# Kernel tuning notes

Hardware: AMD Instinct MI355X
Metric: run time of the kernel (lower is better)

The kernel has to match this reference:

```python
import jax, jax.numpy as jnp
import numpy as np

V, D, H, L, B, T = 32000, 1024, 16, 4, 2, 2048
DH = D // H
F = 4 * D
EPS = 1e-5


def setup_inputs() -> dict:
    key = jax.random.key(0)
    ks = jax.random.split(key, 16)
    s = 0.02
    n = lambda k, shape: (jax.random.normal(k, shape, jnp.float32) * s)
    inp = {
        "idx": jax.random.randint(ks[0], (B, T), 0, V, dtype=jnp.int64),
        "tok_emb": n(ks[1], (V, D)),
        "pos_emb": n(ks[2], (1, T, D)),
        # per-layer stacked params; Linear weights stored as (in, out)
        "Wq": n(ks[3], (L, D, D)), "bq": jnp.zeros((L, D)),
        "Wk": n(ks[4], (L, D, D)), "bk": jnp.zeros((L, D)),
        "Wv": n(ks[5], (L, D, D)), "bv": jnp.zeros((L, D)),
        "Wo": n(ks[6], (L, D, D)), "bo": jnp.zeros((L, D)),
        "ln1_g": jnp.ones((L, D)), "ln1_b": jnp.zeros((L, D)),
        "W1": n(ks[7], (L, D, F)), "b1": jnp.zeros((L, F)),
        "W2": n(ks[8], (L, F, D)), "b2": jnp.zeros((L, D)),
        "ln2_g": jnp.ones((L, D)), "ln2_b": jnp.zeros((L, D)),
        "lnf_g": jnp.ones((D,)), "lnf_b": jnp.zeros((D,)),
        "lm_W": n(ks[9], (D, V)),
    }
    return inp


def _ln(x, g, b):
    m = jnp.mean(x, axis=-1, keepdims=True)
    v = jnp.mean(jnp.square(x - m), axis=-1, keepdims=True)
    return (x - m) * jax.lax.rsqrt(v + EPS) * g + b


def _band_attn(x, Wq, bq, Wk, bk, Wv, bv, Wo, bo):
    # width-3 causal band: query t attends to keys {t, t-1, t-2}
    b_, t_, _ = x.shape
    q = (x @ Wq + bq).reshape(b_, t_, H, DH)
    k = (x @ Wk + bk).reshape(b_, t_, H, DH)
    v = (x @ Wv + bv).reshape(b_, t_, H, DH)

    def shift(a, o):  # align key at position t-o with query t
        return jnp.pad(a, ((0, 0), (o, 0), (0, 0), (0, 0)))[:, :t_]

    ks_ = jnp.stack([shift(k, o) for o in range(3)], axis=-2)  # (B,T,H,3,DH)
    vs_ = jnp.stack([shift(v, o) for o in range(3)], axis=-2)
    scale = 1.0 / np.sqrt(DH)
    scores = jnp.einsum('bthd,bthod->btho', q, ks_) * scale       # (B,T,H,3)
    pos = jnp.arange(t_)[None, :, None, None]
    off = jnp.arange(3)[None, None, None, :]
    scores = jnp.where(pos >= off, scores, -jnp.inf)
    p = jax.nn.softmax(scores, axis=-1)
    y = jnp.einsum('btho,bthod->bthd', p, vs_).reshape(b_, t_, D)
    return y @ Wo + bo


def reference(idx, tok_emb, pos_emb, Wq, bq, Wk, bk, Wv, bv, Wo, bo,
              ln1_g, ln1_b, W1, b1, W2, b2, ln2_g, ln2_b, lnf_g, lnf_b, lm_W):
    t_ = idx.shape[1]
    x = tok_emb[idx] + pos_emb[:, :t_, :]
    for i in range(L):
        h = _ln(x, ln1_g[i], ln1_b[i])
        x = x + _band_attn(h, Wq[i], bq[i], Wk[i], bk[i], Wv[i], bv[i], Wo[i], bo[i])
        h = _ln(x, ln2_g[i], ln2_b[i])
        h = jax.nn.gelu(h @ W1[i] + b1[i], approximate=False) @ W2[i] + b2[i]
        x = x + h
    x = _ln(x, lnf_g, lnf_b)
    logits = x @ lm_W
    return logits
```

## Files before the change

kernel.cpp:

```cpp
#include <hip/hip_runtime.h>
#include <cstdint>
#include <cstddef>

#define MROWS   4096
#define TSEQ    2048
#define DMODEL  1024
#define NHEAD   16
#define FFN     4096
#define NVOCAB  32000
#define NLAYER  4

typedef float  f32x4  __attribute__((ext_vector_type(4)));
typedef __bf16 bf16x8 __attribute__((ext_vector_type(8)));

#define VMCNT(n) asm volatile("s_waitcnt vmcnt(" #n ")" ::: "memory")

__device__ __forceinline__ unsigned short f2bf(float f) {
    unsigned u = __builtin_bit_cast(unsigned, f);
    u += 0x7fffu + ((u >> 16) & 1u);
    return (unsigned short)(u >> 16);
}
__device__ __forceinline__ float bf2f(unsigned short u) {
    return __builtin_bit_cast(float, (unsigned)u << 16);
}

__device__ __forceinline__ float gelu_exact(float v) {
    return 0.5f * v * (1.0f + erff(v * 0.7071067811865476f));
}

__global__ __launch_bounds__(256) void embed_kernel(const int* __restrict__ idx,
                                                    const float* __restrict__ tok,
                                                    const float* __restrict__ pos,
                                                    float* __restrict__ x) {
    int row = blockIdx.x, tid = threadIdx.x;
    int token = idx[row];
    int t = row & (TSEQ - 1);
    float4 a = ((const float4*)(tok + (size_t)token * DMODEL))[tid];
    float4 p = ((const float4*)(pos + (size_t)t * DMODEL))[tid];
    a.x += p.x; a.y += p.y; a.z += p.z; a.w += p.w;
    ((float4*)(x + (size_t)row * DMODEL))[tid] = a;
}

__global__ __launch_bounds__(256) void ln_kernel(const float* __restrict__ x,
                                                 const float* __restrict__ g,
                                                 const float* __restrict__ b,
                                                 unsigned short* __restrict__ out) {
    int row = blockIdx.x, tid = threadIdx.x;
    float4 v = ((const float4*)(x + (size_t)row * DMODEL))[tid];
    float s1 = v.x + v.y + v.z + v.w;
    float s2 = v.x * v.x + v.y * v.y + v.z * v.z + v.w * v.w;
    for (int s = 32; s; s >>= 1) { s1 += __shfl_xor(s1, s); s2 += __shfl_xor(s2, s); }
    __shared__ float red[8];
    int lane = tid & 63, w = tid >> 6;
    if (lane == 0) { red[w] = s1; red[4 + w] = s2; }
    __syncthreads();
    s1 = red[0] + red[1] + red[2] + red[3];
    s2 = red[4] + red[5] + red[6] + red[7];
    float mean = s1 * (1.0f / DMODEL);
    float var  = s2 * (1.0f / DMODEL) - mean * mean;
    float rs   = rsqrtf(var + 1e-5f);
    float4 gv = ((const float4*)g)[tid];
    float4 bv = ((const float4*)b)[tid];
    size_t o = (size_t)row * DMODEL + tid * 4;
    out[o + 0] = f2bf((v.x - mean) * rs * gv.x + bv.x);
    out[o + 1] = f2bf((v.y - mean) * rs * gv.y + bv.y);
    out[o + 2] = f2bf((v.z - mean) * rs * gv.z + bv.z);
    out[o + 3] = f2bf((v.w - mean) * rs * gv.w + bv.w);
}

__global__ __launch_bounds__(256) void transpose_bf16(const float* __restrict__ W,
                                                      unsigned short* __restrict__ WT,
                                                      int K, int ldW) {
    __shared__ float tile[64][65];
    int n0 = blockIdx.x * 64, k0 = blockIdx.y * 64;
    int tid = threadIdx.x;
    int lr4 = tid & 15;
    int rw  = tid >> 4;
#pragma unroll
    for (int p = 0; p < 4; ++p) {
        int k = rw + p * 16;
        float4 v = *(const float4*)(W + (size_t)(k0 + k) * ldW + n0 + lr4 * 4);
        tile[k][lr4 * 4 + 0] = v.x;
        tile[k][lr4 * 4 + 1] = v.y;
        tile[k][lr4 * 4 + 2] = v.z;
        tile[k][lr4 * 4 + 3] = v.w;
    }
    __syncthreads();
    int kc = tid & 15;
    int nr = tid >> 4;
#pragma unroll
    for (int p = 0; p < 4; ++p) {
        int n = nr + p * 16;
        ushort4 o;
        o.x = f2bf(tile[kc * 4 + 0][n]);
        o.y = f2bf(tile[kc * 4 + 1][n]);
        o.z = f2bf(tile[kc * 4 + 2][n]);
        o.w = f2bf(tile[kc * 4 + 3][n]);
        *(ushort4*)(WT + (size_t)(n0 + n) * K + k0 + kc * 4) = o;
    }
}

__global__ __launch_bounds__(256) void transpose_qkv(const float* __restrict__ Wq,
                                                     const float* __restrict__ Wk,
                                                     const float* __restrict__ Wv,
                                                     unsigned short* __restrict__ WT) {
    __shared__ float tile[64][65];
    const float* W = (blockIdx.z == 0) ? Wq : (blockIdx.z == 1) ? Wk : Wv;
    unsigned short* dst = WT + (size_t)blockIdx.z * DMODEL * DMODEL;
    int n0 = blockIdx.x * 64, k0 = blockIdx.y * 64;
    int tid = threadIdx.x;
    int lr4 = tid & 15, rw = tid >> 4;
#pragma unroll
    for (int p = 0; p < 4; ++p) {
        int k = rw + p * 16;
        float4 v = *(const float4*)(W + (size_t)(k0 + k) * DMODEL + n0 + lr4 * 4);
        tile[k][lr4 * 4 + 0] = v.x;
        tile[k][lr4 * 4 + 1] = v.y;
        tile[k][lr4 * 4 + 2] = v.z;
        tile[k][lr4 * 4 + 3] = v.w;
    }
    __syncthreads();
    int kc = tid & 15, nr = tid >> 4;
#pragma unroll
    for (int p = 0; p < 4; ++p) {
        int n = nr + p * 16;
        ushort4 o;
        o.x = f2bf(tile[kc * 4 + 0][n]);
        o.y = f2bf(tile[kc * 4 + 1][n]);
        o.z = f2bf(tile[kc * 4 + 2][n]);
        o.w = f2bf(tile[kc * 4 + 3][n]);
        *(ushort4*)(dst + (size_t)(n0 + n) * DMODEL + k0 + kc * 4) = o;
    }
}

__global__ __launch_bounds__(256) void pack_qkv_bias(const float* __restrict__ bq,
                                                     const float* __restrict__ bk,
                                                     const float* __restrict__ bv,
                                                     float* __restrict__ dst) {
    int i = blockIdx.x * 256 + threadIdx.x;
    int l = i / 3072, c = i % 3072;
    float v = (c < 1024) ? bq[l * 1024 + c]
            : (c < 2048) ? bk[l * 1024 + c - 1024]
                         : bv[l * 1024 + c - 2048];
    dst[i] = v;
}

__global__ __launch_bounds__(256) void attn_kernel(const unsigned short* __restrict__ qkv,
                                                   unsigned short* __restrict__ y) {
    int wid  = (blockIdx.x * 256 + threadIdx.x) >> 6;
    int lane = threadIdx.x & 63;
    int h = wid & (NHEAD - 1);
    int row = wid >> 4;
    int t = row & (TSEQ - 1);
    const unsigned short* base = qkv + (size_t)row * 3072 + h * 64;
    float qd = bf2f(base[lane]);
    float d0 = qd * bf2f(base[1024 + lane]);
    float d1 = (t >= 1) ? qd * bf2f(base[1024 - 3072 + lane]) : 0.0f;
    float d2 = (t >= 2) ? qd * bf2f(base[1024 - 6144 + lane]) : 0.0f;
    for (int s = 32; s; s >>= 1) {
        d0 += __shfl_xor(d0, s); d1 += __shfl_xor(d1, s); d2 += __shfl_xor(d2, s);
    }
    d0 *= 0.125f; d1 *= 0.125f; d2 *= 0.125f;
    float m = d0;
    if (t >= 1) m = fmaxf(m, d1);
    if (t >= 2) m = fmaxf(m, d2);
    float p0 = expf(d0 - m);
    float p1 = (t >= 1) ? expf(d1 - m) : 0.0f;
    float p2 = (t >= 2) ? expf(d2 - m) : 0.0f;
    float den = p0 + p1 + p2;
    float v0 = bf2f(base[2048 + lane]);
    float v1 = (t >= 1) ? bf2f(base[2048 - 3072 + lane]) : 0.0f;
    float v2 = (t >= 2) ? bf2f(base[2048 - 6144 + lane]) : 0.0f;
    float yv = (p0 * v0 + p1 * v1 + p2 * v2) / den;
    y[(size_t)row * DMODEL + h * 64 + lane] = f2bf(yv);
}

template <int EPI>
__global__ __launch_bounds__(512, 2) void gemm256(const unsigned short* __restrict__ A,
                                                  const unsigned short* __restrict__ BT,
                                                  const float* __restrict__ bias,
                                                  const float* __restrict__ res,
                                                  float* __restrict__ outF,
                                                  unsigned short* __restrict__ outB,
                                                  int M, int N, int K, int ldc) {
    __shared__ unsigned short As[4][256 * 32];
    __shared__ unsigned short Bs[4][256 * 32];
    const int tid = threadIdx.x;
    const int lane = tid & 63, wid = tid >> 6;
    const int wr = wid >> 2, wc = wid & 3;
    const int lr = lane & 15, kq = lane >> 4;

    const int nbm = M >> 8;
    const int nwg = gridDim.x;
    int orig = blockIdx.x;
    int q8 = nwg >> 3, r8 = nwg & 7;
    int xcd = orig & 7, lin = orig >> 3;
    int wg = (xcd < r8 ? xcd * (q8 + 1) : r8 * (q8 + 1) + (xcd - r8) * q8) + lin;
    int bm = wg % nbm, bn = wg / nbm;

    const unsigned short* Ab = A + (size_t)bm * 256 * K;
    const unsigned short* Bb = BT + (size_t)bn * 256 * K;

    int sOff[2];
#pragma unroll
    for (int i = 0; i < 2; ++i) {
        int pc = i * 512 + tid;
        int row = pc >> 2;
        int cl = (pc & 3) ^ (row & 3);
        sOff[i] = row * K + cl * 8;
    }

#define STAGE_A256(T) do {                                                                     \
    unsigned short* d_ = &As[(T) & 3][0];                                                      \
    __builtin_amdgcn_global_load_lds(                                                          \
        (const __attribute__((address_space(1))) void*)(Ab + sOff[0] + (T) * 32),              \
        (__attribute__((address_space(3))) void*)(d_ + (size_t)tid * 8), 16, 0, 0);            \
    __builtin_amdgcn_global_load_lds(                                                          \
        (const __attribute__((address_space(1))) void*)(Ab + sOff[1] + (T) * 32),              \
        (__attribute__((address_space(3))) void*)(d_ + (size_t)(tid + 512) * 8), 16, 0, 0);    \
} while (0)
#define STAGE_B256(T) do {                                                                     \
    unsigned short* d_ = &Bs[(T) & 3][0];                                                      \
    __builtin_amdgcn_global_load_lds(                                                          \
        (const __attribute__((address_space(1))) void*)(Bb + sOff[0] + (T) * 32),              \
        (__attribute__((address_space(3))) void*)(d_ + (size_t)tid * 8), 16, 0, 0);            \
    __builtin_amdgcn_global_load_lds(                                                          \
        (const __attribute__((address_space(1))) void*)(Bb + sOff[1] + (T) * 32),              \
        (__attribute__((address_space(3))) void*)(d_ + (size_t)(tid + 512) * 8), 16, 0, 0);    \
} while (0)

    int aOff[8], bOff[4];
#pragma unroll
    for (int m = 0; m < 8; ++m)
        aOff[m] = (wr * 128 + m * 16 + lr) * 32 + ((kq ^ (lr & 3)) * 8);
#pragma unroll
    for (int n = 0; n < 4; ++n)
        bOff[n] = (wc * 64 + n * 16 + lr) * 32 + ((kq ^ (lr & 3)) * 8);

    f32x4 acc[8][4] = {};
    const int nt = K >> 5;

    STAGE_A256(0); STAGE_B256(0);
    STAGE_A256(1); STAGE_B256(1);
    STAGE_A256(2); STAGE_B256(2);

#define GTILE256(T, WN, PF) do {                                                               \
    VMCNT(WN);                                                                                 \
    __builtin_amdgcn_s_barrier();                                                              \
    const unsigned short* sA_ = &As[(T) & 3][0];                                               \
    const unsigned short* sB_ = &Bs[(T) & 3][0];                                               \
    bf16x8 bfr[4], afl[4], afh[4];                                                             \
    _Pragma("unroll") for (int n = 0; n < 4; ++n) bfr[n] = *(const bf16x8*)(sB_ + bOff[n]);    \
    _Pragma("unroll") for (int m = 0; m < 4; ++m) afl[m] = *(const bf16x8*)(sA_ + aOff[m]);    \
    _Pragma("unroll") for (int m = 0; m < 4; ++m) afh[m] = *(const bf16x8*)(sA_ + aOff[4 + m]);\
    if (PF) { STAGE_A256((T) + 3); STAGE_B256((T) + 3); }                                      \
    __builtin_amdgcn_s_setprio(1);                                                             \
    _Pragma("unroll") for (int m = 0; m < 4; ++m)                                              \
        _Pragma("unroll") for (int n = 0; n < 4; ++n)                                          \
            acc[m][n] = __builtin_amdgcn_mfma_f32_16x16x32_bf16(afl[m], bfr[n], acc[m][n], 0, 0, 0); \
    _Pragma("unroll") for (int m = 0; m < 4; ++m)                                              \
        _Pragma("unroll") for (int n = 0; n < 4; ++n)                                          \
            acc[4 + m][n] = __builtin_amdgcn_mfma_f32_16x16x32_bf16(afh[m], bfr[n], acc[4 + m][n], 0, 0, 0); \
    __builtin_amdgcn_s_setprio(0);                                                             \
} while (0)

    int t = 0;
    for (; t < nt - 3; ++t) GTILE256(t, 8, true);
    GTILE256(t, 8, false); ++t;
    GTILE256(t, 4, false); ++t;
    GTILE256(t, 0, false);

    const int row0 = bm * 256 + wr * 128;
    const int col0 = bn * 256 + wc * 64;
#pragma unroll
    for (int m = 0; m < 8; ++m) {
#pragma unroll
        for (int n = 0; n < 4; ++n) {
            int col = col0 + n * 16 + lr;
            int rbase = row0 + m * 16 + kq * 4;
            float bb = bias ? bias[col] : 0.0f;
#pragma unroll
            for (int j = 0; j < 4; ++j) {
                size_t off = (size_t)(rbase + j) * ldc + col;
                float v = acc[m][n][j] + bb;
                if (EPI == 1) v += res[off];
                if (EPI == 2)      outB[off] = f2bf(gelu_exact(v));
                else if (EPI == 3) outB[off] = f2bf(v);
                else               outF[off] = v;
            }
        }
    }
#undef GTILE256
#undef STAGE_A256
#undef STAGE_B256
}

template <int EPI>
__global__ __launch_bounds__(512, 4) void gemm128(const unsigned short* __restrict__ A,
                                                  const unsigned short* __restrict__ BT,
                                                  const float* __restrict__ bias,
                                                  const float* __restrict__ res,
                                                  float* __restrict__ outF,
                                                  unsigned short* __restrict__ outB,
                                                  int M, int N, int K, int ldc) {
    __shared__ unsigned short As[4][128 * 32];
    __shared__ unsigned short Bs[4][128 * 32];
    const int tid = threadIdx.x;
    const int lane = tid & 63, wid = tid >> 6;
    const int wr = wid >> 2, wc = wid & 3;
    const int lr = lane & 15, kq = lane >> 4;

    const int nbm = M >> 7;
    const int nwg = gridDim.x;
    int orig = blockIdx.x;
    int q8 = nwg >> 3, r8 = nwg & 7;
    int xcd = orig & 7, lin = orig >> 3;
    int wg = (xcd < r8 ? xcd * (q8 + 1) : r8 * (q8 + 1) + (xcd - r8) * q8) + lin;
    int bm = wg % nbm, bn = wg / nbm;

    const unsigned short* Ab = A + (size_t)bm * 128 * K;
    const unsigned short* Bb = BT + (size_t)bn * 128 * K;

    int sOff;
    {
        int row = tid >> 2;
        int cl = (tid & 3) ^ (row & 3);
        sOff = row * K + cl * 8;
    }

#define STAGE_AB128(T) do {                                                                    \
    __builtin_amdgcn_global_load_lds(                                                          \
        (const __attribute__((address_space(1))) void*)(Ab + sOff + (T) * 32),                 \
        (__attribute__((address_space(3))) void*)(&As[(T) & 3][0] + (size_t)tid * 8), 16, 0, 0); \
    __builtin_amdgcn_global_load_lds(                                                          \
        (const __attribute__((address_space(1))) void*)(Bb + sOff + (T) * 32),                 \
        (__attribute__((address_space(3))) void*)(&Bs[(T) & 3][0] + (size_t)tid * 8), 16, 0, 0); \
} while (0)

    int aOff[4], bOff[2];
#pragma unroll
    for (int m = 0; m < 4; ++m)
        aOff[m] = (wr * 64 + m * 16 + lr) * 32 + ((kq ^ (lr & 3)) * 8);
#pragma unroll
    for (int n = 0; n < 2; ++n)
        bOff[n] = (wc * 32 + n * 16 + lr) * 32 + ((kq ^ (lr & 3)) * 8);

    f32x4 acc[4][2] = {};
    const int nt = K >> 5;

    STAGE_AB128(0); STAGE_AB128(1); STAGE_AB128(2);

#define GTILE128(T, WN, PF) do {                                                               \
    VMCNT(WN);                                                                                 \
    __builtin_amdgcn_s_barrier();                                                              \
    const unsigned short* sA_ = &As[(T) & 3][0];                                               \
    const unsigned short* sB_ = &Bs[(T) & 3][0];                                               \
    bf16x8 bfr[2], af[4];                                                                      \
    _Pragma("unroll") for (int n = 0; n < 2; ++n) bfr[n] = *(const bf16x8*)(sB_ + bOff[n]);    \
    _Pragma("unroll") for (int m = 0; m < 4; ++m) af[m] = *(const bf16x8*)(sA_ + aOff[m]);     \
    if (PF) STAGE_AB128((T) + 3);                                                              \
    __builtin_amdgcn_s_setprio(1);                                                             \
    _Pragma("unroll") for (int m = 0; m < 4; ++m)                                              \
        _Pragma("unroll") for (int n = 0; n < 2; ++n)                                          \
            acc[m][n] = __builtin_amdgcn_mfma_f32_16x16x32_bf16(af[m], bfr[n], acc[m][n], 0, 0, 0); \
    __builtin_amdgcn_s_setprio(0);                                                             \
} while (0)

    int t = 0;
    for (; t < nt - 3; ++t) GTILE128(t, 4, true);
    GTILE128(t, 4, false); ++t;
    GTILE128(t, 2, false); ++t;
    GTILE128(t, 0, false);

    const int row0 = bm * 128 + wr * 64;
    const int col0 = bn * 128 + wc * 32;
#pragma unroll
    for (int m = 0; m < 4; ++m) {
#pragma unroll
        for (int n = 0; n < 2; ++n) {
            int col = col0 + n * 16 + lr;
            int rbase = row0 + m * 16 + kq * 4;
            float bb = bias ? bias[col] : 0.0f;
#pragma unroll
            for (int j = 0; j < 4; ++j) {
                size_t off = (size_t)(rbase + j) * ldc + col;
                float v = acc[m][n][j] + bb;
                if (EPI == 1) v += res[off];
                if (EPI == 2)      outB[off] = f2bf(gelu_exact(v));
                else if (EPI == 3) outB[off] = f2bf(v);
                else               outF[off] = v;
            }
        }
    }
#undef GTILE128
#undef STAGE_AB128
}

extern "C" void kernel_launch(void* const* d_in, const int* in_sizes, int n_in,
                              void* d_out, int out_size, void* d_ws, size_t ws_size,
                              hipStream_t stream) {
    const int*   idx  = (const int*)d_in[0];
    const float* tok  = (const float*)d_in[1];
    const float* pos  = (const float*)d_in[2];
    const float* Wq   = (const float*)d_in[3];
    const float* bq   = (const float*)d_in[4];
    const float* Wk   = (const float*)d_in[5];
    const float* bk   = (const float*)d_in[6];
    const float* Wv   = (const float*)d_in[7];
    const float* bv   = (const float*)d_in[8];
    const float* Wo   = (const float*)d_in[9];
    const float* bo   = (const float*)d_in[10];
    const float* ln1g = (const float*)d_in[11];
    const float* ln1b = (const float*)d_in[12];
    const float* W1   = (const float*)d_in[13];
    const float* b1   = (const float*)d_in[14];
    const float* W2   = (const float*)d_in[15];
    const float* b2   = (const float*)d_in[16];
    const float* ln2g = (const float*)d_in[17];
    const float* ln2b = (const float*)d_in[18];
    const float* lnfg = (const float*)d_in[19];
    const float* lnfb = (const float*)d_in[20];
    const float* lmW  = (const float*)d_in[21];

    const bool bigws = ws_size >= (92ull << 20);

    char* ws = (char*)d_ws;
    unsigned short* wbuf;
    unsigned short* hbuf;
    unsigned short* ybuf;
    unsigned short* xfbuf;
    float*          bqkv;
    if (bigws) {
        wbuf  = (unsigned short*)(ws);
        hbuf  = (unsigned short*)(ws + (63ull << 20));
        ybuf  = (unsigned short*)(ws + (71ull << 20));
        xfbuf = (unsigned short*)(ws + (79ull << 20));
        bqkv  = (float*)(ws + (87ull << 20));
    } else {
        wbuf  = (unsigned short*)(ws);
        hbuf  = (unsigned short*)(ws + (16u << 20));
        ybuf  = (unsigned short*)(ws + (24u << 20));
        xfbuf = (unsigned short*)(ws + (32u << 20));
        bqkv  = (float*)(ws + (40u << 20));
    }

    float* outF = (float*)d_out;
    float* xbuf = outF;
    unsigned short* qkv = (unsigned short*)((char*)d_out + (16ull << 20));
    unsigned short* hidden = (unsigned short*)((char*)d_out + (64ull << 20));

    embed_kernel<<<MROWS, 256, 0, stream>>>(idx, tok, pos, xbuf);
    pack_qkv_bias<<<(NLAYER * 3072) / 256, 256, 0, stream>>>(bq, bk, bv, bqkv);

    for (int l = 0; l < NLAYER; l++) {
        const size_t wl = (size_t)l * DMODEL * DMODEL;
        ln_kernel<<<MROWS, 256, 0, stream>>>(xbuf, ln1g + l * DMODEL, ln1b + l * DMODEL, hbuf);

        transpose_qkv<<<dim3(16, 16, 3), 256, 0, stream>>>(Wq + wl, Wk + wl, Wv + wl, wbuf);
        gemm256<3><<<dim3((3072 / 256) * (MROWS / 256)), 512, 0, stream>>>(
            hbuf, wbuf, bqkv + l * 3072, nullptr, nullptr, qkv, MROWS, 3072, DMODEL, 3072);

        attn_kernel<<<MROWS * NHEAD / 4, 256, 0, stream>>>(qkv, ybuf);

        transpose_bf16<<<dim3(16, 16), 256, 0, stream>>>(Wo + wl, wbuf, DMODEL, DMODEL);
        gemm128<1><<<dim3((DMODEL / 128) * (MROWS / 128)), 512, 0, stream>>>(
            ybuf, wbuf, bo + l * DMODEL, xbuf, xbuf, nullptr, MROWS, DMODEL, DMODEL, DMODEL);

        ln_kernel<<<MROWS, 256, 0, stream>>>(xbuf, ln2g + l * DMODEL, ln2b + l * DMODEL, hbuf);

        transpose_bf16<<<dim3(FFN / 64, DMODEL / 64), 256, 0, stream>>>(W1 + (size_t)l * DMODEL * FFN, wbuf, DMODEL, FFN);
        gemm256<2><<<dim3((FFN / 256) * (MROWS / 256)), 512, 0, stream>>>(
            hbuf, wbuf, b1 + l * FFN, nullptr, nullptr, hidden, MROWS, FFN, DMODEL, FFN);

        transpose_bf16<<<dim3(DMODEL / 64, FFN / 64), 256, 0, stream>>>(W2 + (size_t)l * FFN * DMODEL, wbuf, FFN, DMODEL);
        gemm128<1><<<dim3((DMODEL / 128) * (MROWS / 128)), 512, 0, stream>>>(
            hidden, wbuf, b2 + l * DMODEL, xbuf, xbuf, nullptr, MROWS, DMODEL, FFN, DMODEL);
    }

    ln_kernel<<<MROWS, 256, 0, stream>>>(xbuf, lnfg, lnfb, xfbuf);

    if (bigws) {
        transpose_bf16<<<dim3(NVOCAB / 64, DMODEL / 64), 256, 0, stream>>>(lmW, wbuf, DMODEL, NVOCAB);
        gemm256<0><<<dim3((NVOCAB / 256) * (MROWS / 256)), 512, 0, stream>>>(
            xfbuf, wbuf, nullptr, nullptr, outF, nullptr, MROWS, NVOCAB, DMODEL, NVOCAB);
    } else {
        const int NCHUNK = 6400;
        for (int c = 0; c < NVOCAB / NCHUNK; c++) {
            int n0 = c * NCHUNK;
            transpose_bf16<<<dim3(NCHUNK / 64, DMODEL / 64), 256, 0, stream>>>(lmW + n0, wbuf, DMODEL, NVOCAB);
            gemm256<0><<<dim3((NCHUNK / 256) * (MROWS / 256)), 512, 0, stream>>>(
                xfbuf, wbuf, nullptr, nullptr, outF + n0, nullptr, MROWS, NCHUNK, DMODEL, NVOCAB);
        }
    }
}
```

Baseline: 1.369 ms.

## Restructure gemm256 into double-buffered 64-K ping-pong pipeline with new LDS swizzle

After: 1.331 ms, median of 2. -2.8%, faster.

```diff
diff --git a/kernel.cpp b/kernel.cpp
--- a/kernel.cpp
+++ b/kernel.cpp
@@ -14,6 +14,7 @@
 typedef __bf16 bf16x8 __attribute__((ext_vector_type(8)));
 
 #define VMCNT(n) asm volatile("s_waitcnt vmcnt(" #n ")" ::: "memory")
+#define LGKM0()  asm volatile("s_waitcnt lgkmcnt(0)" ::: "memory")
 
 __device__ __forceinline__ unsigned short f2bf(float f) {
     unsigned u = __builtin_bit_cast(unsigned, f);
@@ -183,8 +184,8 @@
                                                   float* __restrict__ outF,
                                                   unsigned short* __restrict__ outB,
                                                   int M, int N, int K, int ldc) {
-    __shared__ unsigned short As[4][256 * 32];
-    __shared__ unsigned short Bs[4][256 * 32];
+    __shared__ unsigned short As[2][2][8192];
+    __shared__ unsigned short Bs[2][2][8192];
     const int tid = threadIdx.x;
     const int lane = tid & 63, wid = tid >> 6;
     const int wr = wid >> 2, wc = wid & 3;
@@ -201,74 +202,114 @@
     const unsigned short* Ab = A + (size_t)bm * 256 * K;
     const unsigned short* Bb = BT + (size_t)bn * 256 * K;
 
-    int sOff[2];
-#pragma unroll
-    for (int i = 0; i < 2; ++i) {
-        int pc = i * 512 + tid;
-        int row = pc >> 2;
-        int cl = (pc & 3) ^ (row & 3);
-        sOff[i] = row * K + cl * 8;
-    }
-
-#define STAGE_A256(T) do {                                                                     \
-    unsigned short* d_ = &As[(T) & 3][0];                                                      \
+    int sG0, sG1;
+    {
+        int pc0 = tid,        l0 = pc0 >> 3, s0 = pc0 & 7;
+        int pc1 = 512 + tid,  l1 = pc1 >> 3, s1 = pc1 & 7;
+        sG0 = (l0 * 2 + (s0 >> 2)) * K + (((s0 & 3) ^ (l0 & 3)) * 8);
+        sG1 = (l1 * 2 + (s1 >> 2)) * K + (((s1 & 3) ^ (l1 & 3)) * 8);
+    }
+
+#define STAGE256(REGION, GBASE, TT, KH) do {                                                   \
     __builtin_amdgcn_global_load_lds(                                                          \
-        (const __attribute__((address_space(1))) void*)(Ab + sOff[0] + (T) * 32),              \
-        (__attribute__((address_space(3))) void*)(d_ + (size_t)tid * 8), 16, 0, 0);            \
+        (const __attribute__((address_space(1))) void*)((GBASE) + sG0 + (TT) * 64 + (KH) * 32),\
+        (__attribute__((address_space(3))) void*)((REGION) + (size_t)tid * 8), 16, 0, 0);      \
     __builtin_amdgcn_global_load_lds(                                                          \
-        (const __attribute__((address_space(1))) void*)(Ab + sOff[1] + (T) * 32),              \
-        (__attribute__((address_space(3))) void*)(d_ + (size_t)(tid + 512) * 8), 16, 0, 0);    \
+        (const __attribute__((address_space(1))) void*)((GBASE) + sG1 + (TT) * 64 + (KH) * 32),\
+        (__attribute__((address_space(3))) void*)((REGION) + (size_t)(512 + tid) * 8), 16, 0, 0);\
 } while (0)
-#define STAGE_B256(T) do {                                                                     \
-    unsigned short* d_ = &Bs[(T) & 3][0];                                                      \
-    __builtin_amdgcn_global_load_lds(                                                          \
-        (const __attribute__((address_space(1))) void*)(Bb + sOff[0] + (T) * 32),              \
-        (__attribute__((address_space(3))) void*)(d_ + (size_t)tid * 8), 16, 0, 0);            \
-    __builtin_amdgcn_global_load_lds(                                                          \
-        (const __attribute__((address_space(1))) void*)(Bb + sOff[1] + (T) * 32),              \
-        (__attribute__((address_space(3))) void*)(d_ + (size_t)(tid + 512) * 8), 16, 0, 0);    \
-} while (0)
-
-    int aOff[8], bOff[4];
-#pragma unroll
-    for (int m = 0; m < 8; ++m)
-        aOff[m] = (wr * 128 + m * 16 + lr) * 32 + ((kq ^ (lr & 3)) * 8);
-#pragma unroll
-    for (int n = 0; n < 4; ++n)
-        bOff[n] = (wc * 64 + n * 16 + lr) * 32 + ((kq ^ (lr & 3)) * 8);
+
+    const int slot = ((lane & 1) << 2) | (kq ^ ((lr >> 1) & 3));
+    const int laneOff = ((lr >> 1) << 6) + slot * 8;
+    const int aBase = wr * 4096 + laneOff;
+    const int bBase = wc * 2048 + laneOff;
 
     f32x4 acc[8][4] = {};
-    const int nt = K >> 5;
-
-    STAGE_A256(0); STAGE_B256(0);
-    STAGE_A256(1); STAGE_B256(1);
-    STAGE_A256(2); STAGE_B256(2);
-
-#define GTILE256(T, WN, PF) do {                                                               \
-    VMCNT(WN);                                                                                 \
-    __builtin_amdgcn_s_barrier();                                                              \
-    const unsigned short* sA_ = &As[(T) & 3][0];                                               \
-    const unsigned short* sB_ = &Bs[(T) & 3][0];                                               \
-    bf16x8 bfr[4], afl[4], afh[4];                                                             \
-    _Pragma("unroll") for (int n = 0; n < 4; ++n) bfr[n] = *(const bf16x8*)(sB_ + bOff[n]);    \
-    _Pragma("unroll") for (int m = 0; m < 4; ++m) afl[m] = *(const bf16x8*)(sA_ + aOff[m]);    \
-    _Pragma("unroll") for (int m = 0; m < 4; ++m) afh[m] = *(const bf16x8*)(sA_ + aOff[4 + m]);\
-    if (PF) { STAGE_A256((T) + 3); STAGE_B256((T) + 3); }                                      \
-    __builtin_amdgcn_s_setprio(1);                                                             \
-    _Pragma("unroll") for (int m = 0; m < 4; ++m)                                              \
-        _Pragma("unroll") for (int n = 0; n < 4; ++n)                                          \
-            acc[m][n] = __builtin_amdgcn_mfma_f32_16x16x32_bf16(afl[m], bfr[n], acc[m][n], 0, 0, 0); \
-    _Pragma("unroll") for (int m = 0; m < 4; ++m)                                              \
-        _Pragma("unroll") for (int n = 0; n < 4; ++n)                                          \
-            acc[4 + m][n] = __builtin_amdgcn_mfma_f32_16x16x32_bf16(afh[m], bfr[n], acc[4 + m][n], 0, 0, 0); \
-    __builtin_amdgcn_s_setprio(0);                                                             \
-} while (0)
-
-    int t = 0;
-    for (; t < nt - 3; ++t) GTILE256(t, 8, true);
-    GTILE256(t, 8, false); ++t;
-    GTILE256(t, 4, false); ++t;
-    GTILE256(t, 0, false);
+    const int nt = K >> 6;
+
+    STAGE256(&As[0][0][0], Ab, 0, 0);
+    STAGE256(&Bs[0][0][0], Bb, 0, 0);
+    STAGE256(&As[0][1][0], Ab, 0, 1);
+    STAGE256(&Bs[0][1][0], Bb, 0, 1);
+    VMCNT(4);
+    __builtin_amdgcn_s_barrier();
+
+    for (int t = 0; t < nt; ++t) {
+        const int buf = t & 1;
+        const bool pf = (t + 1) < nt;
+        const unsigned short* A0 = &As[buf][0][0];
+        const unsigned short* A1 = &As[buf][1][0];
+        const unsigned short* B0 = &Bs[buf][0][0];
+        const unsigned short* B1 = &Bs[buf][1][0];
+        unsigned short* nA0 = &As[buf ^ 1][0][0];
+        unsigned short* nA1 = &As[buf ^ 1][1][0];
+        unsigned short* nB0 = &Bs[buf ^ 1][0][0];
+        unsigned short* nB1 = &Bs[buf ^ 1][1][0];
+
+        bf16x8 a[8], b0, b1;
+
+#pragma unroll
+        for (int m = 0; m < 8; ++m) a[m] = *(const bf16x8*)(A0 + aBase + m * 512);
+        b0 = *(const bf16x8*)(B0 + bBase + 0 * 512);
+        b1 = *(const bf16x8*)(B0 + bBase + 1 * 512);
+        if (pf) STAGE256(nA0, Ab, t + 1, 0);
+        __builtin_amdgcn_s_barrier();
+        LGKM0();
+        __builtin_amdgcn_s_setprio(1);
+#pragma unroll
+        for (int m = 0; m < 8; ++m) {
+            acc[m][0] = __builtin_amdgcn_mfma_f32_16x16x32_bf16(a[m], b0, acc[m][0], 0, 0, 0);
+            acc[m][1] = __builtin_amdgcn_mfma_f32_16x16x32_bf16(a[m], b1, acc[m][1], 0, 0, 0);
+        }
+        __builtin_amdgcn_s_setprio(0);
+        __builtin_amdgcn_s_barrier();
+
+        b0 = *(const bf16x8*)(B0 + bBase + 2 * 512);
+        b1 = *(const bf16x8*)(B0 + bBase + 3 * 512);
+        if (pf) STAGE256(nB0, Bb, t + 1, 0);
+        __builtin_amdgcn_s_barrier();
+        LGKM0();
+        __builtin_amdgcn_s_setprio(1);
+#pragma unroll
+        for (int m = 0; m < 8; ++m) {
+            acc[m][2] = __builtin_amdgcn_mfma_f32_16x16x32_bf16(a[m], b0, acc[m][2], 0, 0, 0);
+            acc[m][3] = __builtin_amdgcn_mfma_f32_16x16x32_bf16(a[m], b1, acc[m][3], 0, 0, 0);
+        }
+        __builtin_amdgcn_s_setprio(0);
+        if (pf) VMCNT(4); else VMCNT(0);
+        __builtin_amdgcn_s_barrier();
+
+#pragma unroll
+        for (int m = 0; m < 8; ++m) a[m] = *(const bf16x8*)(A1 + aBase + m * 512);
+        b0 = *(const bf16x8*)(B1 + bBase + 0 * 512);
+        b1 = *(const bf16x8*)(B1 + bBase + 1 * 512);
+        if (pf) STAGE256(nA1, Ab, t + 1, 1);
+        __builtin_amdgcn_s_barrier();
+        LGKM0();
+        __builtin_amdgcn_s_setprio(1);
+#pragma unroll
+        for (int m = 0; m < 8; ++m) {
+            acc[m][0] = __builtin_amdgcn_mfma_f32_16x16x32_bf16(a[m], b0, acc[m][0], 0, 0, 0);
+            acc[m][1] = __builtin_amdgcn_mfma_f32_16x16x32_bf16(a[m], b1, acc[m][1], 0, 0, 0);
+        }
+        __builtin_amdgcn_s_setprio(0);
+        __builtin_amdgcn_s_barrier();
+
+        b0 = *(const bf16x8*)(B1 + bBase + 2 * 512);
+        b1 = *(const bf16x8*)(B1 + bBase + 3 * 512);
+        if (pf) STAGE256(nB1, Bb, t + 1, 1);
+        __builtin_amdgcn_s_barrier();
+        LGKM0();
+        __builtin_amdgcn_s_setprio(1);
+#pragma unroll
+        for (int m = 0; m < 8; ++m) {
+            acc[m][2] = __builtin_amdgcn_mfma_f32_16x16x32_bf16(a[m], b0, acc[m][2], 0, 0, 0);
+            acc[m][3] = __builtin_amdgcn_mfma_f32_16x16x32_bf16(a[m], b1, acc[m][3], 0, 0, 0);
+        }
+        __builtin_amdgcn_s_setprio(0);
+        if (pf) VMCNT(4);
+        __builtin_amdgcn_s_barrier();
+    }
 
     const int row0 = bm * 256 + wr * 128;
     const int col0 = bn * 256 + wc * 64;
@@ -290,9 +331,7 @@
             }
         }
     }
-#undef GTILE256
-#undef STAGE_A256
-#undef STAGE_B256
+#undef STAGE256
 }
 
 template <int EPI>
@@ -323,9 +362,8 @@
 
     int sOff;
     {
-        int row = tid >> 2;
-        int cl = (tid & 3) ^ (row & 3);
-        sOff = row * K + cl * 8;
+        int l0 = tid >> 3, s0 = tid & 7;
+        sOff = (l0 * 2 + (s0 >> 2)) * K + (((s0 & 3) ^ (l0 & 3)) * 8);
     }
 
 #define STAGE_AB128(T) do {                                                                    \
@@ -337,13 +375,13 @@
         (__attribute__((address_space(3))) void*)(&Bs[(T) & 3][0] + (size_t)tid * 8), 16, 0, 0); \
 } while (0)
 
+    const int slot = ((lane & 1) << 2) | (kq ^ ((lr >> 1) & 3));
+    const int laneOff = ((lr >> 1) << 6) + slot * 8;
     int aOff[4], bOff[2];
 #pragma unroll
-    for (int m = 0; m < 4; ++m)
-        aOff[m] = (wr * 64 + m * 16 + lr) * 32 + ((kq ^ (lr & 3)) * 8);
-#pragma unroll
-    for (int n = 0; n < 2; ++n)
-        bOff[n] = (wc * 32 + n * 16 + lr) * 32 + ((kq ^ (lr & 3)) * 8);
+    for (int m = 0; m < 4; ++m) aOff[m] = wr * 2048 + m * 512 + laneOff;
+#pragma unroll
+    for (int n = 0; n < 2; ++n) bOff[n] = wc * 1024 + n * 512 + laneOff;
 
     f32x4 acc[4][2] = {};
     const int nt = K >> 5;
```
